# Performance work log

Measured on AMD Instinct MI355X. Metric: run time of the kernel, lower is better.

## Reference

```python
import jax, jax.numpy as jnp
import numpy as np

N, K = 50000, 10      # nodes, sampled neighbors (num_sample)
V, F = 200000, 128    # embedding table rows, input_dim
H = 64                # hidden per direction (hidden_dim=128, bidirectional)


def setup_inputs() -> dict:
    key = jax.random.key(0)
    ks = jax.random.split(key, 12)
    s = 1.0 / np.sqrt(H)  # torch LSTM init: U(-1/sqrt(H), 1/sqrt(H))
    u = lambda k, shape: jax.random.uniform(k, shape, jnp.float32, -s, s)
    return {
        "neigh_idx": jax.random.randint(ks[0], (N, K), 0, V),
        "embed_table": jax.random.normal(ks[1], (V, F), jnp.float32) * 0.02,
        # forward-direction LSTM params (torch gate order: i, f, g, o)
        "Wih_f": u(ks[2], (4 * H, F)), "Whh_f": u(ks[3], (4 * H, H)),
        "bih_f": u(ks[4], (4 * H,)),   "bhh_f": u(ks[5], (4 * H,)),
        # backward-direction LSTM params
        "Wih_b": u(ks[6], (4 * H, F)), "Whh_b": u(ks[7], (4 * H, H)),
        "bih_b": u(ks[8], (4 * H,)),   "bhh_b": u(ks[9], (4 * H,)),
    }


def _lstm_scan(x, Wih, Whh, bih, bhh):
    """x: [N,K,F] -> hidden outputs [N,K,H] (single direction)."""
    n = x.shape[0]
    # precompute input projections for all steps: [N,K,4H]
    xg = jnp.einsum('nkf,gf->nkg', x, Wih) + bih + bhh
    h0 = jnp.zeros((n, H), x.dtype)
    c0 = jnp.zeros((n, H), x.dtype)

    def step(carry, xt):
        h, c = carry
        gates = xt + h @ Whh.T
        i, f, g, o = jnp.split(gates, 4, axis=-1)
        i = jax.nn.sigmoid(i)
        f = jax.nn.sigmoid(f)
        g = jnp.tanh(g)
        o = jax.nn.sigmoid(o)
        c = f * c + i * g
        h = o * jnp.tanh(c)
        return (h, c), h

    _, hs = jax.lax.scan(step, (h0, c0), jnp.swapaxes(xg, 0, 1))  # [K,N,H]
    return jnp.swapaxes(hs, 0, 1)


def reference(neigh_idx, embed_table, Wih_f, Whh_f, bih_f, bhh_f,
              Wih_b, Whh_b, bih_b, bhh_b):
    x = embed_table[neigh_idx]  # gather: [N,K,F]
    # forward direction: last-step hidden
    h_f = _lstm_scan(x, Wih_f, Whh_f, bih_f, bhh_f)[:, -1, :]
    # backward direction processes reversed sequence; torch output[:, -1] of the
    # backward stream is its hidden after processing only element K-1 (step 0).
    h_b = _lstm_scan(x[:, ::-1, :], Wih_b, Whh_b, bih_b, bhh_b)[:, 0, :]
    return jnp.concatenate([h_f, h_b], axis=-1)  # [N, 2H]
```

## Files before the change

kernel.cpp:

```cpp
#include <hip/hip_runtime.h>
#include <hip/hip_bf16.h>


#define NN 50000
#define KK 10
#define FF 128
#define HH 64

#define WS_WIH_F 0
#define WS_WHH_F 32768
#define WS_WIH_B 49152

#define NPB 32
#define HS 72

typedef __bf16 bf16x8 __attribute__((ext_vector_type(8)));
typedef float f32x4 __attribute__((ext_vector_type(4)));

__device__ __forceinline__ float fast_sig(float x) {
    float e = exp2f(x * -1.44269504f);
    return __builtin_amdgcn_rcpf(1.0f + e);
}
__device__ __forceinline__ float fast_tanh(float x) {
    float xx = fminf(fmaxf(x, -15.0f), 15.0f);
    float e = exp2f(xx * 2.88539008f);
    return (e - 1.0f) * __builtin_amdgcn_rcpf(e + 1.0f);
}

__global__ void cvt_weights_kernel(const float* __restrict__ Wih_f,
                                   const float* __restrict__ Whh_f,
                                   const float* __restrict__ Wih_b,
                                   __bf16* __restrict__ ws) {
    int i = blockIdx.x * 256 + threadIdx.x;
    ws[WS_WIH_F + i] = (__bf16)Wih_f[i];
    if (i < 16384) ws[WS_WHH_F + i] = (__bf16)Whh_f[i];
    ws[WS_WIH_B + i] = (__bf16)Wih_b[i];
}

__global__ __launch_bounds__(256, 2) void lstm_agg_kernel(
    const int* __restrict__ nidx,
    const float* __restrict__ tab,
    const float* __restrict__ bih_f,
    const float* __restrict__ bhh_f,
    const float* __restrict__ bih_b,
    const float* __restrict__ bhh_b,
    const __bf16* __restrict__ ws,
    float* __restrict__ out)
{
    __shared__ __bf16 x_lds[2][NPB * FF];
    __shared__ __bf16 h_lds[2][NPB * HS];
    __shared__ int    gq[NPB][KK];

    const int tid  = threadIdx.x;
    const int w    = tid >> 6;
    const int lane = tid & 63;
    const int q    = lane >> 4;
    const int c    = lane & 15;
    const int koff = q * 8;
    const int node_base = blockIdx.x * NPB;
    const int sw = (c & 7) << 4;

    const int srow  = tid >> 3;
    const int spart = tid & 7;
    const int swW   = (srow & 7) << 4;

    for (int i = tid; i < NPB * KK; i += 256) {
        int r = i / KK, k = i - r * KK;
        int node = min(node_base + r, NN - 1);
        gq[r][k] = nidx[node * KK + k];
    }

    f32x4 G[4];
    auto stage_load = [&](int kidx) {
        const float* src = tab + (size_t)gq[srow][kidx] * FF + spart * 16;
#pragma unroll
        for (int j = 0; j < 4; ++j) G[j] = *(const f32x4*)(src + j * 4);
    };
    auto stage_write = [&](int b) {
        bf16x8 v0, v1;
#pragma unroll
        for (int e = 0; e < 4; ++e) {
            v0[e]     = (__bf16)G[0][e];
            v0[4 + e] = (__bf16)G[1][e];
            v1[e]     = (__bf16)G[2][e];
            v1[4 + e] = (__bf16)G[3][e];
        }
        char* row = (char*)(x_lds[b] + srow * FF);
        *(bf16x8*)(row + ((spart * 32)      ^ swW)) = v0;
        *(bf16x8*)(row + ((spart * 32 + 16) ^ swW)) = v1;
    };

    __syncthreads();
    stage_load(0);

    bf16x8 bWih[4][4], bWhh[4][2];
#pragma unroll
    for (int g = 0; g < 4; ++g) {
        int row = (g * 4 + w) * 16 + c;
#pragma unroll
        for (int kk = 0; kk < 4; ++kk)
            bWih[g][kk] = *(const bf16x8*)(ws + WS_WIH_F + row * FF + kk * 32 + koff);
#pragma unroll
        for (int kk = 0; kk < 2; ++kk)
            bWhh[g][kk] = *(const bf16x8*)(ws + WS_WHH_F + row * HH + kk * 32 + koff);
    }
    float bias[4];
#pragma unroll
    for (int g = 0; g < 4; ++g) {
        int u = g * 64 + w * 16 + c;
        bias[g] = bih_f[u] + bhh_f[u];
    }

    stage_write(0);
    __syncthreads();

    f32x4 acc[4][2];
    float cst[2][4];
#pragma unroll
    for (int r = 0; r < 2; ++r)
#pragma unroll
        for (int e = 0; e < 4; ++e) cst[r][e] = 0.0f;

    for (int k = 0; k < KK; ++k) {
        const int cur = k & 1;
        if (k + 1 < KK) stage_load(k + 1);

#pragma unroll
        for (int g = 0; g < 4; ++g)
#pragma unroll
            for (int r = 0; r < 2; ++r)
                acc[g][r] = (f32x4){bias[g], bias[g], bias[g], bias[g]};

        const char* xb = (const char*)x_lds[cur];
#pragma unroll
        for (int r = 0; r < 2; ++r) {
            const char* rp = xb + (r * 16 + c) * 256;
            bf16x8 xa[4];
#pragma unroll
            for (int kk = 0; kk < 4; ++kk)
                xa[kk] = *(const bf16x8*)(rp + ((kk * 64 + q * 16) ^ sw));
#pragma unroll
            for (int g = 0; g < 4; ++g)
#pragma unroll
                for (int kk = 0; kk < 4; ++kk)
                    acc[g][r] = __builtin_amdgcn_mfma_f32_16x16x32_bf16(
                        xa[kk], bWih[g][kk], acc[g][r], 0, 0, 0);
        }

        if (k > 0) {
            const __bf16* hb = h_lds[(k - 1) & 1];
#pragma unroll
            for (int r = 0; r < 2; ++r) {
                bf16x8 ha[2];
#pragma unroll
                for (int kk = 0; kk < 2; ++kk)
                    ha[kk] = *(const bf16x8*)(hb + (r * 16 + c) * HS + kk * 32 + koff);
#pragma unroll
                for (int g = 0; g < 4; ++g)
#pragma unroll
                    for (int kk = 0; kk < 2; ++kk)
                        acc[g][r] = __builtin_amdgcn_mfma_f32_16x16x32_bf16(
                            ha[kk], bWhh[g][kk], acc[g][r], 0, 0, 0);
            }
        }

        const bool last = (k == KK - 1);
        __bf16* hw = h_lds[k & 1];
#pragma unroll
        for (int r = 0; r < 2; ++r)
#pragma unroll
            for (int reg = 0; reg < 4; ++reg) {
                float gi = fast_sig(acc[0][r][reg]);
                float gf = fast_sig(acc[1][r][reg]);
                float gg = fast_tanh(acc[2][r][reg]);
                float go = fast_sig(acc[3][r][reg]);
                float cn = gf * cst[r][reg] + gi * gg;
                cst[r][reg] = cn;
                float h = go * fast_tanh(cn);
                hw[(r * 16 + q * 4 + reg) * HS + w * 16 + c] = (__bf16)h;
                if (last) {
                    int node = node_base + r * 16 + q * 4 + reg;
                    if (node < NN) out[(size_t)node * 128 + w * 16 + c] = h;
                }
            }

        if (k + 1 < KK) stage_write(cur ^ 1);
        __syncthreads();
    }

    {
        const int gb[3] = {0, 2, 3};
        bf16x8 bW[3][4];
        float  bb[3];
#pragma unroll
        for (int j = 0; j < 3; ++j) {
            int row = (gb[j] * 4 + w) * 16 + c;
#pragma unroll
            for (int kk = 0; kk < 4; ++kk)
                bW[j][kk] = *(const bf16x8*)(ws + WS_WIH_B + row * FF + kk * 32 + koff);
            int u = gb[j] * 64 + w * 16 + c;
            bb[j] = bih_b[u] + bhh_b[u];
        }
        const char* xb = (const char*)x_lds[(KK - 1) & 1];
#pragma unroll
        for (int r = 0; r < 2; ++r) {
            f32x4 a0 = (f32x4){bb[0], bb[0], bb[0], bb[0]};
            f32x4 a1 = (f32x4){bb[1], bb[1], bb[1], bb[1]};
            f32x4 a2 = (f32x4){bb[2], bb[2], bb[2], bb[2]};
            const char* rp = xb + (r * 16 + c) * 256;
            bf16x8 xa[4];
#pragma unroll
            for (int kk = 0; kk < 4; ++kk)
                xa[kk] = *(const bf16x8*)(rp + ((kk * 64 + q * 16) ^ sw));
#pragma unroll
            for (int kk = 0; kk < 4; ++kk) {
                a0 = __builtin_amdgcn_mfma_f32_16x16x32_bf16(xa[kk], bW[0][kk], a0, 0, 0, 0);
                a1 = __builtin_amdgcn_mfma_f32_16x16x32_bf16(xa[kk], bW[1][kk], a1, 0, 0, 0);
                a2 = __builtin_amdgcn_mfma_f32_16x16x32_bf16(xa[kk], bW[2][kk], a2, 0, 0, 0);
            }
#pragma unroll
            for (int reg = 0; reg < 4; ++reg) {
                float gi = fast_sig(a0[reg]);
                float gg = fast_tanh(a1[reg]);
                float go = fast_sig(a2[reg]);
                float hb2 = go * fast_tanh(gi * gg);
                int node = node_base + r * 16 + q * 4 + reg;
                if (node < NN) out[(size_t)node * 128 + 64 + w * 16 + c] = hb2;
            }
        }
    }
}

extern "C" void kernel_launch(void* const* d_in, const int* in_sizes, int n_in,
                              void* d_out, int out_size, void* d_ws, size_t ws_size,
                              hipStream_t stream) {
    const int*   nidx  = (const int*)d_in[0];
    const float* tab   = (const float*)d_in[1];
    const float* Wih_f = (const float*)d_in[2];
    const float* Whh_f = (const float*)d_in[3];
    const float* bih_f = (const float*)d_in[4];
    const float* bhh_f = (const float*)d_in[5];
    const float* Wih_b = (const float*)d_in[6];
    const float* bih_b = (const float*)d_in[8];
    const float* bhh_b = (const float*)d_in[9];
    __bf16* ws  = (__bf16*)d_ws;
    float*  out = (float*)d_out;

    hipLaunchKernelGGL(cvt_weights_kernel, dim3(32768 / 256), dim3(256), 0, stream,
                       Wih_f, Whh_f, Wih_b, ws);

    const int blocks = (NN + NPB - 1) / NPB;
    hipLaunchKernelGGL(lstm_agg_kernel, dim3(blocks), dim3(256), 0, stream,
                       nidx, tab, bih_f, bhh_f, bih_b, bhh_b, ws, out);
}
```

Measured before the change: 254.2 us.

## Pack gate activations into float2 math, raise occupancy, prioritize MFMA phase

Rewrites the per-step gate nonlinearities to work on pairs of values with float2 vectors, so the compiler can emit packed FP32 ops. Drops the clamp in tanh and uses a 1-2/(e+1) form. Raises launch bounds to 3 blocks per CU, unrolls the time loop by 2, and raises wave priority around the MFMA section. The aim is to cut VALU cost in the activation phase and hide latency with more resident waves. The cost is register pressure from the higher occupancy target, which could cause spills.

```diff
diff --git a/kernel.cpp b/kernel.cpp
--- a/kernel.cpp
+++ b/kernel.cpp
@@ -16,15 +16,28 @@
 
 typedef __bf16 bf16x8 __attribute__((ext_vector_type(8)));
 typedef float f32x4 __attribute__((ext_vector_type(4)));
+typedef float f32x2 __attribute__((ext_vector_type(2)));
 
 __device__ __forceinline__ float fast_sig(float x) {
     float e = exp2f(x * -1.44269504f);
     return __builtin_amdgcn_rcpf(1.0f + e);
 }
 __device__ __forceinline__ float fast_tanh(float x) {
-    float xx = fminf(fmaxf(x, -15.0f), 15.0f);
-    float e = exp2f(xx * 2.88539008f);
-    return (e - 1.0f) * __builtin_amdgcn_rcpf(e + 1.0f);
+    float e = exp2f(x * 2.88539008f);
+    return 1.0f - 2.0f * __builtin_amdgcn_rcpf(e + 1.0f);
+}
+__device__ __forceinline__ f32x2 sig2(f32x2 x) {
+    f32x2 t = x * -1.44269504f;
+    f32x2 e = {exp2f(t.x), exp2f(t.y)};
+    f32x2 d = e + 1.0f;
+    return (f32x2){__builtin_amdgcn_rcpf(d.x), __builtin_amdgcn_rcpf(d.y)};
+}
+__device__ __forceinline__ f32x2 tanh2(f32x2 x) {
+    f32x2 t = x * 2.88539008f;
+    f32x2 e = {exp2f(t.x), exp2f(t.y)};
+    f32x2 d = e + 1.0f;
+    f32x2 r = {__builtin_amdgcn_rcpf(d.x), __builtin_amdgcn_rcpf(d.y)};
+    return 1.0f - 2.0f * r;
 }
 
 __global__ void cvt_weights_kernel(const float* __restrict__ Wih_f,
@@ -37,7 +50,7 @@
     ws[WS_WIH_B + i] = (__bf16)Wih_b[i];
 }
 
-__global__ __launch_bounds__(256, 2) void lstm_agg_kernel(
+__global__ __launch_bounds__(256, 3) void lstm_agg_kernel(
     const int* __restrict__ nidx,
     const float* __restrict__ tab,
     const float* __restrict__ bih_f,
@@ -121,6 +134,7 @@
 #pragma unroll
         for (int e = 0; e < 4; ++e) cst[r][e] = 0.0f;
 
+#pragma unroll 2
     for (int k = 0; k < KK; ++k) {
         const int cur = k & 1;
         if (k + 1 < KK) stage_load(k + 1);
@@ -131,6 +145,7 @@
             for (int r = 0; r < 2; ++r)
                 acc[g][r] = (f32x4){bias[g], bias[g], bias[g], bias[g]};
 
+        __builtin_amdgcn_s_setprio(1);
         const char* xb = (const char*)x_lds[cur];
 #pragma unroll
         for (int r = 0; r < 2; ++r) {
@@ -163,24 +178,33 @@
                             ha[kk], bWhh[g][kk], acc[g][r], 0, 0, 0);
             }
         }
+        __builtin_amdgcn_s_setprio(0);
 
         const bool last = (k == KK - 1);
         __bf16* hw = h_lds[k & 1];
 #pragma unroll
         for (int r = 0; r < 2; ++r)
 #pragma unroll
-            for (int reg = 0; reg < 4; ++reg) {
-                float gi = fast_sig(acc[0][r][reg]);
-                float gf = fast_sig(acc[1][r][reg]);
-                float gg = fast_tanh(acc[2][r][reg]);
-                float go = fast_sig(acc[3][r][reg]);
-                float cn = gf * cst[r][reg] + gi * gg;
-                cst[r][reg] = cn;
-                float h = go * fast_tanh(cn);
-                hw[(r * 16 + q * 4 + reg) * HS + w * 16 + c] = (__bf16)h;
+            for (int p = 0; p < 2; ++p) {
+                f32x2 ai = {acc[0][r][2 * p], acc[0][r][2 * p + 1]};
+                f32x2 af = {acc[1][r][2 * p], acc[1][r][2 * p + 1]};
+                f32x2 ag = {acc[2][r][2 * p], acc[2][r][2 * p + 1]};
+                f32x2 ao = {acc[3][r][2 * p], acc[3][r][2 * p + 1]};
+                f32x2 gi = sig2(ai);
+                f32x2 gf = sig2(af);
+                f32x2 gg = tanh2(ag);
+                f32x2 go = sig2(ao);
+                f32x2 cc = {cst[r][2 * p], cst[r][2 * p + 1]};
+                f32x2 cn = gf * cc + gi * gg;
+                cst[r][2 * p]     = cn.x;
+                cst[r][2 * p + 1] = cn.y;
+                f32x2 h = go * tanh2(cn);
+                hw[(r * 16 + q * 4 + 2 * p)     * HS + w * 16 + c] = (__bf16)h.x;
+                hw[(r * 16 + q * 4 + 2 * p + 1) * HS + w * 16 + c] = (__bf16)h.y;
                 if (last) {
-                    int node = node_base + r * 16 + q * 4 + reg;
-                    if (node < NN) out[(size_t)node * 128 + w * 16 + c] = h;
+                    int node = node_base + r * 16 + q * 4 + 2 * p;
+                    if (node < NN)     out[(size_t)node * 128 + w * 16 + c] = h.x;
+                    if (node + 1 < NN) out[(size_t)(node + 1) * 128 + w * 16 + c] = h.y;
                 }
             }
 
```

Result: slower. 401.0 us (+57.8%).
